# Performance work log

Measured on AMD Instinct MI355X. Metric: run time of the kernel, lower is better.

## Reference

```python
import jax, jax.numpy as jnp
import numpy as np

P = 22   # matrix size (number of variables)
K = 1    # number of full column sweeps
B = 16384  # batch of precision matrices


def _one_pass(Theta, W, Wcol):
    """One sweep over all p columns (Sherman-Morrison style rank-1 updates).
    Theta, W: (B, p, p); Wcol: (p-1, p-1) learned column map."""
    p = Theta.shape[-1]

    def body(carry, col):
        Theta, W = carry
        # indices of all rows/cols except `col` (length p-1)
        minus = jnp.arange(p - 1)
        minus = minus + (minus >= col).astype(minus.dtype)

        theta_22 = Theta[:, col, col]                      # (B,)
        theta_12 = Theta[:, minus, col]                    # (B, p-1)
        W_11 = W[:, minus[:, None], minus[None, :]]        # (B, p-1, p-1)
        w_22 = W[:, col, col]                              # (B,)
        w_12 = W[:, minus, col]                            # (B, p-1)

        # inv(Theta_11) via block-inverse identity: W_11 - w_12 w_12^T / w_22
        inv_Theta_11 = W_11 - (w_12[:, :, None] * w_12[:, None, :]) / w_22[:, None, None]

        # learned column update: Linear(p-1, p-1, bias=False) -> x @ W^T
        theta_12_next = theta_12 @ Wcol.T                  # (B, p-1)

        Av = jnp.einsum('bij,bj->bi', inv_Theta_11, theta_12_next)   # (B, p-1)
        schur = jnp.einsum('bi,bi->b', theta_12_next, Av)            # (B,)
        # gy = theta_22 - schur; theta_22_next = gy + schur (as in source)
        theta_22_next = (theta_22 - schur) + schur

        # Theta <- Theta + Delta (equivalent to setting the updated entries)
        Theta = Theta.at[:, col, col].set(theta_22_next)
        Theta = Theta.at[:, minus, col].set(theta_12_next)
        Theta = Theta.at[:, col, minus].set(theta_12_next)

        # update_W_from_Theta (all writes detached in the original)
        w_22_next = 1.0 / (theta_22_next - schur)                        # (B,)
        w_12_next = -w_22_next[:, None] * Av                             # (B, p-1)
        W_11_next = inv_Theta_11 + (w_12_next[:, :, None] * w_12_next[:, None, :]) / w_22_next[:, None, None]
        sg = jax.lax.stop_gradient
        W = W.at[:, minus[:, None], minus[None, :]].set(sg(W_11_next))
        W = W.at[:, minus, col].set(sg(w_12_next))
        W = W.at[:, col, minus].set(sg(w_12_next))
        W = W.at[:, col, col].set(sg(w_22_next))
        return (Theta, W), None

    (Theta, W), _ = jax.lax.scan(body, (Theta, W), jnp.arange(p))
    return Theta, W


def _forward(Theta, Wcol):
    # W = inv(Theta), detached (torch: .detach())
    W = jax.lax.stop_gradient(jnp.linalg.inv(Theta))
    for _ in range(K):
        Theta, W = _one_pass(Theta, W, Wcol)
    return Theta


def setup_inputs() -> dict:
    key = jax.random.key(0)
    k1, k2 = jax.random.split(key)
    A = jax.random.normal(k1, (B, P, P), dtype=jnp.float32) / np.float32(np.sqrt(P))
    # SPD, well-conditioned precision matrices
    Theta = A @ jnp.swapaxes(A, -1, -2) + jnp.eye(P, dtype=jnp.float32)
    # small init keeps theta_22 - schur > 0 (valid Schur complement)
    Wcol = 0.01 * jax.random.normal(k2, (P - 1, P - 1), dtype=jnp.float32)
    return {"Theta": Theta, "Wcol": Wcol}


def reference(Theta, Wcol):
    return _forward(Theta, Wcol)
```

## Files before the change

### kernel.cpp

```cpp
#include <hip/hip_runtime.h>


#define PP 22
#define PM 21
#define MAT 484
#define TB 8
#define TILE_FLOATS (TB * MAT)
#define TILE_BYTES  (TILE_FLOATS * 4)

typedef const __attribute__((address_space(1))) void* gas_ptr;
typedef __attribute__((address_space(3))) void* las_ptr;

__global__ __launch_bounds__(64, 4)
void spodnet_sweep(const float* __restrict__ theta_in,
                   const float* __restrict__ wcol,
                   float* __restrict__ theta_out)
{
    __shared__ float lds[TILE_FLOATS];
    const int lane = threadIdx.x;
    const int g = lane >> 3;
    const int k = lane & 7;

    const long b0 = (long)blockIdx.x * TB;
    const float* gin  = theta_in  + b0 * MAT;
    float*       gout = theta_out + b0 * MAT;

    {
        const char* src = (const char*)gin;
        #pragma unroll
        for (int it = 0; it < 15; ++it) {
            __builtin_amdgcn_global_load_lds(
                (gas_ptr)(src + it * 1024 + lane * 16),
                (las_ptr)((char*)lds + it * 1024),
                16, 0, 0);
        }
        if (lane < 8) {
            __builtin_amdgcn_global_load_lds(
                (gas_ptr)(src + 15360 + lane * 16),
                (las_ptr)((char*)lds + 15360),
                16, 0, 0);
        }
    }

    float w0[PM], w1[PM], w2[PM];
    {
        const int r0 = k, r1 = k + 8, r2 = (k < 5) ? (k + 16) : 20;
        #pragma unroll
        for (int j = 0; j < PM; ++j) {
            w0[j] = wcol[r0 * PM + j];
            w1[j] = wcol[r1 * PM + j];
            w2[j] = wcol[r2 * PM + j];
        }
    }

    asm volatile("s_waitcnt vmcnt(0)" ::: "memory");
    __builtin_amdgcn_sched_barrier(0);

    float* M = &lds[g * MAT];

    #pragma unroll
    for (int c = 0; c < PP; ++c) {
        float f[PP];
        {
            const float2* row = reinterpret_cast<const float2*>(&M[c * PP]);
            #pragma unroll
            for (int h = 0; h < 11; ++h) {
                float2 t = row[h];
                f[2 * h]     = t.x;
                f[2 * h + 1] = t.y;
            }
        }

        float a0 = 0.f, a1 = 0.f, a2 = 0.f;
        float b0a = 0.f, b1a = 0.f, b2a = 0.f;
        #pragma unroll
        for (int j = 0; j < PM; ++j) {
            const int mj = j + (j >= c ? 1 : 0);
            if (j < 11) {
                a0 = fmaf(w0[j], f[mj], a0);
                a1 = fmaf(w1[j], f[mj], a1);
                a2 = fmaf(w2[j], f[mj], a2);
            } else {
                b0a = fmaf(w0[j], f[mj], b0a);
                b1a = fmaf(w1[j], f[mj], b1a);
                b2a = fmaf(w2[j], f[mj], b2a);
            }
        }
        a0 += b0a; a1 += b1a; a2 += b2a;

        const int mi0 = k      + (k      >= c ? 1 : 0);
        const int mi1 = k + 8  + (k + 8  >= c ? 1 : 0);
        const int mi2 = k + 16 + (k + 16 >= c ? 1 : 0);
        M[mi0 * PP + c] = a0;
        M[mi1 * PP + c] = a1;
        if (k < 5) M[mi2 * PP + c] = a2;
        if (mi0 < c) M[c * PP + mi0] = a0;
        if (mi1 < c) M[c * PP + mi1] = a1;
        if (k < 5 && mi2 < c) M[c * PP + mi2] = a2;
    }

    {
        const float4* l4 = reinterpret_cast<const float4*>(lds);
        float4* g4 = reinterpret_cast<float4*>(gout);
        #pragma unroll
        for (int it = 0; it < 15; ++it)
            g4[it * 64 + lane] = l4[it * 64 + lane];
        if (lane < 8)
            g4[960 + lane] = l4[960 + lane];
    }
}

extern "C" void kernel_launch(void* const* d_in, const int* in_sizes, int n_in,
                              void* d_out, int out_size, void* d_ws, size_t ws_size,
                              hipStream_t stream) {
    const float* theta = (const float*)d_in[0];
    const float* wcol  = (const float*)d_in[1];
    float* out = (float*)d_out;

    const int Btot = in_sizes[0] / (PP * PP);
    const int grid = Btot / TB;
    hipLaunchKernelGGL(spodnet_sweep, dim3(grid), dim3(64), 0, stream,
                       theta, wcol, out);
}
```

Baseline: 21.93 us.

## Process two tiles per block with double-buffered LDS staging

Each block now handles two 8-matrix tiles. Both tiles are loaded asynchronously into two LDS buffers up front, and partial vmcnt waits let the sweep of the first tile start while the second tile's loads are still in flight. The Wcol register load is shared by both tiles. The cost is twice the LDS per block and half as many blocks, which reduces the parallelism available to hide latency.

Result: slower. 25.74 us (+17.4%).

```diff
diff --git a/kernel.cpp b/kernel.cpp
--- a/kernel.cpp
+++ b/kernel.cpp
@@ -11,53 +11,39 @@
 typedef const __attribute__((address_space(1))) void* gas_ptr;
 typedef __attribute__((address_space(3))) void* las_ptr;
 
-__global__ __launch_bounds__(64, 4)
-void spodnet_sweep(const float* __restrict__ theta_in,
-                   const float* __restrict__ wcol,
-                   float* __restrict__ theta_out)
+__device__ __forceinline__ void stage_tile(const float* __restrict__ gsrc,
+                                           float* lbuf, int lane)
 {
-    __shared__ float lds[TILE_FLOATS];
-    const int lane = threadIdx.x;
-    const int g = lane >> 3;
-    const int k = lane & 7;
+    const char* src = (const char*)gsrc;
+    #pragma unroll
+    for (int it = 0; it < 15; ++it) {
+        __builtin_amdgcn_global_load_lds(
+            (gas_ptr)(src + it * 1024 + lane * 16),
+            (las_ptr)((char*)lbuf + it * 1024), 16, 0, 0);
+    }
+    if (lane < 8) {
+        __builtin_amdgcn_global_load_lds(
+            (gas_ptr)(src + 15360 + lane * 16),
+            (las_ptr)((char*)lbuf + 15360), 16, 0, 0);
+    }
+}
 
-    const long b0 = (long)blockIdx.x * TB;
-    const float* gin  = theta_in  + b0 * MAT;
-    float*       gout = theta_out + b0 * MAT;
+__device__ __forceinline__ void store_tile(const float* lbuf,
+                                           float* __restrict__ gdst, int lane)
+{
+    const float4* l4 = reinterpret_cast<const float4*>(lbuf);
+    float4* g4 = reinterpret_cast<float4*>(gdst);
+    #pragma unroll
+    for (int it = 0; it < 15; ++it)
+        g4[it * 64 + lane] = l4[it * 64 + lane];
+    if (lane < 8)
+        g4[960 + lane] = l4[960 + lane];
+}
 
-    {
-        const char* src = (const char*)gin;
-        #pragma unroll
-        for (int it = 0; it < 15; ++it) {
-            __builtin_amdgcn_global_load_lds(
-                (gas_ptr)(src + it * 1024 + lane * 16),
-                (las_ptr)((char*)lds + it * 1024),
-                16, 0, 0);
-        }
-        if (lane < 8) {
-            __builtin_amdgcn_global_load_lds(
-                (gas_ptr)(src + 15360 + lane * 16),
-                (las_ptr)((char*)lds + 15360),
-                16, 0, 0);
-        }
-    }
-
-    float w0[PM], w1[PM], w2[PM];
-    {
-        const int r0 = k, r1 = k + 8, r2 = (k < 5) ? (k + 16) : 20;
-        #pragma unroll
-        for (int j = 0; j < PM; ++j) {
-            w0[j] = wcol[r0 * PM + j];
-            w1[j] = wcol[r1 * PM + j];
-            w2[j] = wcol[r2 * PM + j];
-        }
-    }
-
-    asm volatile("s_waitcnt vmcnt(0)" ::: "memory");
-    __builtin_amdgcn_sched_barrier(0);
-
-    float* M = &lds[g * MAT];
-
+__device__ __forceinline__ void sweep_tile(float* M, int k,
+                                           const float* w0, const float* w1,
+                                           const float* w2)
+{
     #pragma unroll
     for (int c = 0; c < PP; ++c) {
         float f[PP];
@@ -98,16 +84,49 @@
         if (mi1 < c) M[c * PP + mi1] = a1;
         if (k < 5 && mi2 < c) M[c * PP + mi2] = a2;
     }
+}
 
+__global__ __launch_bounds__(64)
+void spodnet_sweep(const float* __restrict__ theta_in,
+                   const float* __restrict__ wcol,
+                   float* __restrict__ theta_out)
+{
+    __shared__ float lds[2][TILE_FLOATS];
+    const int lane = threadIdx.x;
+    const int g = lane >> 3;
+    const int k = lane & 7;
+
+    const long t0 = (long)blockIdx.x * 2;
+    const float* ginA = theta_in  + t0 * TILE_FLOATS;
+    const float* ginB = ginA + TILE_FLOATS;
+    float* goutA = theta_out + t0 * TILE_FLOATS;
+    float* goutB = goutA + TILE_FLOATS;
+
+    stage_tile(ginA, lds[0], lane);
+    stage_tile(ginB, lds[1], lane);
+
+    float w0[PM], w1[PM], w2[PM];
     {
-        const float4* l4 = reinterpret_cast<const float4*>(lds);
-        float4* g4 = reinterpret_cast<float4*>(gout);
+        const int r0 = k, r1 = k + 8, r2 = (k < 5) ? (k + 16) : 20;
         #pragma unroll
-        for (int it = 0; it < 15; ++it)
-            g4[it * 64 + lane] = l4[it * 64 + lane];
-        if (lane < 8)
-            g4[960 + lane] = l4[960 + lane];
+        for (int j = 0; j < PM; ++j) {
+            w0[j] = wcol[r0 * PM + j];
+            w1[j] = wcol[r1 * PM + j];
+            w2[j] = wcol[r2 * PM + j];
+        }
     }
+
+    asm volatile("s_waitcnt vmcnt(16)" ::: "memory");
+    __builtin_amdgcn_sched_barrier(0);
+
+    sweep_tile(&lds[0][g * MAT], k, w0, w1, w2);
+    store_tile(lds[0], goutA, lane);
+
+    asm volatile("s_waitcnt vmcnt(16)" ::: "memory");
+    __builtin_amdgcn_sched_barrier(0);
+
+    sweep_tile(&lds[1][g * MAT], k, w0, w1, w2);
+    store_tile(lds[1], goutB, lane);
 }
 
 extern "C" void kernel_launch(void* const* d_in, const int* in_sizes, int n_in,
@@ -118,7 +137,7 @@
     float* out = (float*)d_out;
 
     const int Btot = in_sizes[0] / (PP * PP);
-    const int grid = Btot / TB;
+    const int grid = Btot / (TB * 2);
     hipLaunchKernelGGL(spodnet_sweep, dim3(grid), dim3(64), 0, stream,
                        theta, wcol, out);
 }
```

## Prefetch next row into register double buffer and use nontemporal stores

Applied to the files above, without the earlier changes.

Double-buffers the LDS row reads in registers, loading row c+1 while column c is computed. Only the one element written by the current column is reloaded after the write, and its FMA is deferred to the end of the dot product. This is meant to hide LDS read latency on the serial column chain. The output copy now uses nontemporal stores and the min-blocks launch bound is dropped, which may raise register use.

Measured after the change: 17.72 us (median of 2 runs). 19.2% less time.

```diff
diff --git a/kernel.cpp b/kernel.cpp
--- a/kernel.cpp
+++ b/kernel.cpp
@@ -6,12 +6,13 @@
 #define MAT 484
 #define TB 8
 #define TILE_FLOATS (TB * MAT)
-#define TILE_BYTES  (TILE_FLOATS * 4)
 
 typedef const __attribute__((address_space(1))) void* gas_ptr;
 typedef __attribute__((address_space(3))) void* las_ptr;
+typedef float f32x4 __attribute__((ext_vector_type(4)));
+typedef float f32x2 __attribute__((ext_vector_type(2)));
 
-__global__ __launch_bounds__(64, 4)
+__global__ __launch_bounds__(64)
 void spodnet_sweep(const float* __restrict__ theta_in,
                    const float* __restrict__ wcol,
                    float* __restrict__ theta_out)
@@ -21,9 +22,8 @@
     const int g = lane >> 3;
     const int k = lane & 7;
 
-    const long b0 = (long)blockIdx.x * TB;
-    const float* gin  = theta_in  + b0 * MAT;
-    float*       gout = theta_out + b0 * MAT;
+    const float* gin  = theta_in  + (long)blockIdx.x * TILE_FLOATS;
+    float*       gout = theta_out + (long)blockIdx.x * TILE_FLOATS;
 
     {
         const char* src = (const char*)gin;
@@ -31,14 +31,12 @@
         for (int it = 0; it < 15; ++it) {
             __builtin_amdgcn_global_load_lds(
                 (gas_ptr)(src + it * 1024 + lane * 16),
-                (las_ptr)((char*)lds + it * 1024),
-                16, 0, 0);
+                (las_ptr)((char*)lds + it * 1024), 16, 0, 0);
         }
         if (lane < 8) {
             __builtin_amdgcn_global_load_lds(
                 (gas_ptr)(src + 15360 + lane * 16),
-                (las_ptr)((char*)lds + 15360),
-                16, 0, 0);
+                (las_ptr)((char*)lds + 15360), 16, 0, 0);
         }
     }
 
@@ -58,35 +56,55 @@
 
     float* M = &lds[g * MAT];
 
+    float fb[2][PP];
+    {
+        const f32x2* row = reinterpret_cast<const f32x2*>(&M[0]);
+        #pragma unroll
+        for (int h = 0; h < 11; ++h) {
+            f32x2 t = row[h];
+            fb[0][2 * h] = t.x; fb[0][2 * h + 1] = t.y;
+        }
+    }
+
     #pragma unroll
     for (int c = 0; c < PP; ++c) {
-        float f[PP];
-        {
-            const float2* row = reinterpret_cast<const float2*>(&M[c * PP]);
+        const int cur = c & 1, nxt = cur ^ 1;
+
+        if (c < PP - 1) {
+            const f32x2* row = reinterpret_cast<const f32x2*>(&M[(c + 1) * PP]);
             #pragma unroll
             for (int h = 0; h < 11; ++h) {
-                float2 t = row[h];
-                f[2 * h]     = t.x;
-                f[2 * h + 1] = t.y;
+                f32x2 t = row[h];
+                fb[nxt][2 * h] = t.x; fb[nxt][2 * h + 1] = t.y;
             }
         }
 
         float a0 = 0.f, a1 = 0.f, a2 = 0.f;
-        float b0a = 0.f, b1a = 0.f, b2a = 0.f;
+        float p0 = 0.f, p1 = 0.f, p2 = 0.f;
+        int cnt = 0;
         #pragma unroll
         for (int j = 0; j < PM; ++j) {
+            if (j == c - 1) continue;
             const int mj = j + (j >= c ? 1 : 0);
-            if (j < 11) {
-                a0 = fmaf(w0[j], f[mj], a0);
-                a1 = fmaf(w1[j], f[mj], a1);
-                a2 = fmaf(w2[j], f[mj], a2);
+            const float fv = fb[cur][mj];
+            if ((cnt & 1) == 0) {
+                a0 = fmaf(w0[j], fv, a0);
+                a1 = fmaf(w1[j], fv, a1);
+                a2 = fmaf(w2[j], fv, a2);
             } else {
-                b0a = fmaf(w0[j], f[mj], b0a);
-                b1a = fmaf(w1[j], f[mj], b1a);
-                b2a = fmaf(w2[j], f[mj], b2a);
+                p0 = fmaf(w0[j], fv, p0);
+                p1 = fmaf(w1[j], fv, p1);
+                p2 = fmaf(w2[j], fv, p2);
             }
+            ++cnt;
         }
-        a0 += b0a; a1 += b1a; a2 += b2a;
+        a0 += p0; a1 += p1; a2 += p2;
+        if (c >= 1) {
+            const float fv = fb[cur][c - 1];
+            a0 = fmaf(w0[c - 1], fv, a0);
+            a1 = fmaf(w1[c - 1], fv, a1);
+            a2 = fmaf(w2[c - 1], fv, a2);
+        }
 
         const int mi0 = k      + (k      >= c ? 1 : 0);
         const int mi1 = k + 8  + (k + 8  >= c ? 1 : 0);
@@ -97,16 +115,19 @@
         if (mi0 < c) M[c * PP + mi0] = a0;
         if (mi1 < c) M[c * PP + mi1] = a1;
         if (k < 5 && mi2 < c) M[c * PP + mi2] = a2;
+
+        if (c < PP - 1)
+            fb[nxt][c] = M[(c + 1) * PP + c];
     }
 
     {
-        const float4* l4 = reinterpret_cast<const float4*>(lds);
-        float4* g4 = reinterpret_cast<float4*>(gout);
+        const f32x4* l4 = reinterpret_cast<const f32x4*>(lds);
+        f32x4* g4 = reinterpret_cast<f32x4*>(gout);
         #pragma unroll
         for (int it = 0; it < 15; ++it)
-            g4[it * 64 + lane] = l4[it * 64 + lane];
+            __builtin_nontemporal_store(l4[it * 64 + lane], &g4[it * 64 + lane]);
         if (lane < 8)
-            g4[960 + lane] = l4[960 + lane];
+            __builtin_nontemporal_store(l4[960 + lane], &g4[960 + lane]);
     }
 }
 
```
